# Kernel optimization log

Measured on AMD Instinct MI355X. Metric: run time of the kernel, lower is better.

Reference implementation:

```python
import jax, jax.numpy as jnp
import numpy as np

HEAD_SIZE = 64

def setup_inputs() -> dict:
    key = jax.random.key(0)
    ks = jax.random.split(key, 6)
    B, T, D, H, HS = 4, 2048, 1024, 16, HEAD_SIZE
    s = 1.0 / np.sqrt(D)
    return {
        "x": jax.random.normal(ks[0], (B, T, D), jnp.float32),
        "Wq": jax.random.normal(ks[1], (H, D, HS), jnp.float32) * s,
        "Wk": jax.random.normal(ks[2], (H, D, HS), jnp.float32) * s,
        "Wv": jax.random.normal(ks[3], (H, D, HS), jnp.float32) * s,
        "Wp": jax.random.normal(ks[4], (D, D), jnp.float32) * s,
        "bp": jnp.zeros((D,), jnp.float32),
    }

def reference(x, Wq, Wk, Wv, Wp, bp):
    B, T, D = x.shape
    H, _, HS = Wq.shape
    # per-head projections (bias-free Linears), stacked over heads
    q = jnp.einsum('btd,hde->bhte', x, Wq)
    k = jnp.einsum('btd,hde->bhte', x, Wk)
    v = jnp.einsum('btd,hde->bhte', x, Wv)
    scores = jnp.einsum('bhqe,bhke->bhqk', q, k) / jnp.sqrt(jnp.float32(HS))
    causal = jnp.tril(jnp.ones((T, T), bool))  # mask[:T,:T]
    scores = jnp.where(causal, scores, -jnp.inf)
    w = jax.nn.softmax(scores, axis=-1)  # dropout p=0.0 -> identity
    out = jnp.einsum('bhqk,bhke->bhqe', w, v)
    # concat heads along last dim: [B,T,H*HS] == [B,T,D]
    out = out.transpose(0, 2, 1, 3).reshape(B, T, H * HS)
    return out @ Wp.T + bp  # note: Wp stored as [out,in] like nn.Linear
```

## Files before the change

kernel.cpp:

```cpp
#include <hip/hip_runtime.h>
#include <hip/hip_bf16.h>

typedef unsigned short u16;
typedef unsigned int u32;
typedef __attribute__((ext_vector_type(8))) short short8;
typedef __attribute__((ext_vector_type(4))) float f32x4;

#define B_ 4
#define T_ 2048
#define D_ 1024
#define H_ 16
#define HS_ 64
#define BT (B_*T_)

__device__ __forceinline__ float bf2f(u16 b){ union{u32 u; float f;} v; v.u=((u32)b)<<16; return v.f; }
__device__ __forceinline__ u16 f2bf(float f){
    __hip_bfloat16 h = __float2bfloat16(f);
    union{__hip_bfloat16 h; u16 u;} v; v.h = h; return v.u;
}
__device__ __forceinline__ void split2(float x, u16& h, u16& l){
    u16 hb = f2bf(x);
    float fh = bf2f(hb);
    h = hb; l = f2bf(x - fh);
}
union U4 { u16 s[4]; uint2 v; };
union S8 { u16 s[8]; short8 v; };

#define GLD16(g,l) __builtin_amdgcn_global_load_lds( \
    (__attribute__((address_space(1))) void*)(u16*)(g), \
    (__attribute__((address_space(3))) void*)(l), 16, 0, 0)

__device__ __forceinline__ int swz(int row, int col){
    return row*64 + (((col>>3) ^ (row&7))<<3) + (col&7);
}
#define FCHK(r) (((r)>>1)&3)

#define DPPMV(x, ctrl) __int_as_float(__builtin_amdgcn_update_dpp(0, __float_as_int(x), (ctrl), 0xF, 0xF, true))

__global__ __launch_bounds__(256) void pack_w(const float* __restrict__ Wq,
                                              const float* __restrict__ Wk,
                                              const float* __restrict__ Wv,
                                              u16* __restrict__ Wth,
                                              u16* __restrict__ Wtl)
{
    __shared__ float Tl[64*68];
    const int h = blockIdx.x, dt = blockIdx.y, z = blockIdx.z;
    const float* src = (z==0) ? Wq : ((z==1) ? Wk : Wv);
    const int t = threadIdx.x;
    const int d0 = dt*64;
    #pragma unroll
    for (int i=0;i<4;++i){
        int ci = t + 256*i;
        int dr = ci>>4, ec = ci&15;
        float4 v = *(const float4*)(src + ((size_t)h*D_ + d0+dr)*HS_ + ec*4);
        *(float4*)(Tl + dr*68 + ec*4) = v;
    }
    __syncthreads();
    #pragma unroll
    for (int i=0;i<4;++i){
        int ci = t + 256*i;
        int e = ci>>4, dc = ci&15;
        U4 hh, ll;
        #pragma unroll
        for (int j=0;j<4;++j){
            float f = Tl[(dc*4+j)*68 + e];
            split2(f, hh.s[j], ll.s[j]);
        }
        int n = z*D_ + h*HS_ + e;
        *(uint2*)(Wth + (size_t)n*D_ + d0 + dc*4) = hh.v;
        *(uint2*)(Wtl + (size_t)n*D_ + d0 + dc*4) = ll.v;
    }
}

__global__ __launch_bounds__(256) void gemm_qkv(const float* __restrict__ x,
                                                const u16* __restrict__ Wth,
                                                const u16* __restrict__ Wtl,
                                                float* __restrict__ qo,
                                                u16* __restrict__ kho, u16* __restrict__ klo,
                                                u16* __restrict__ vth, u16* __restrict__ vtl)
{
    __shared__ u16 Ash[128*32], Asl[128*32];
    __shared__ u16 Bsh[128*32], Bsl[128*32];
    const int n0 = blockIdx.x*128, m0 = blockIdx.y*128;
    const int t = threadIdx.x;
    const int w = t>>6, lane = t&63, quad = lane>>4, l16 = lane&15;
    const int wm = (w>>1)*64, wn = (w&1)*64;
    f32x4 acc[4][4];
    #pragma unroll
    for (int i=0;i<4;++i)
        #pragma unroll
        for (int j=0;j<4;++j) acc[i][j] = (f32x4){0.f,0.f,0.f,0.f};
    for (int kt=0; kt<32; ++kt){
        const int k0 = kt*32;
        #pragma unroll
        for (int i=0;i<2;++i){
            int ci = t + 256*i;
            int row = ci>>2, c = ci&3;
            int cs = c ^ FCHK(row);
            GLD16(Wth + (size_t)(n0+row)*D_ + k0 + cs*8, Bsh + ci*8);
            GLD16(Wtl + (size_t)(n0+row)*D_ + k0 + cs*8, Bsl + ci*8);
        }
        #pragma unroll
        for (int i=0;i<4;++i){
            int ci = t + 256*i;
            int row = ci>>3, c4 = ci&7;
            float4 av = *(const float4*)(x + (size_t)(m0+row)*D_ + k0 + c4*4);
            U4 hh, ll;
            split2(av.x, hh.s[0], ll.s[0]); split2(av.y, hh.s[1], ll.s[1]);
            split2(av.z, hh.s[2], ll.s[2]); split2(av.w, hh.s[3], ll.s[3]);
            int off = row*32 + ((((c4>>1) ^ FCHK(row))<<3) | ((c4&1)<<2));
            *(uint2*)(Ash + off) = hh.v;
            *(uint2*)(Asl + off) = ll.v;
        }
        __syncthreads();
        short8 afh[4], afl[4], bfh[4], bfl[4];
        #pragma unroll
        for (int mi=0;mi<4;++mi){
            const int rr = wm+mi*16+l16;
            const int off = rr*32 + ((quad ^ FCHK(rr))<<3);
            afh[mi] = *(const short8*)(Ash + off);
            afl[mi] = *(const short8*)(Asl + off);
        }
        #pragma unroll
        for (int ni=0;ni<4;++ni){
            const int rr = wn+ni*16+l16;
            const int off = rr*32 + ((quad ^ FCHK(rr))<<3);
            bfh[ni] = *(const short8*)(Bsh + off);
            bfl[ni] = *(const short8*)(Bsl + off);
        }
        #pragma unroll
        for (int mi=0;mi<4;++mi)
            #pragma unroll
            for (int ni=0;ni<4;++ni){
                acc[mi][ni] = __builtin_amdgcn_mfma_f32_16x16x32_bf16(afh[mi], bfh[ni], acc[mi][ni], 0,0,0);
                acc[mi][ni] = __builtin_amdgcn_mfma_f32_16x16x32_bf16(afh[mi], bfl[ni], acc[mi][ni], 0,0,0);
                acc[mi][ni] = __builtin_amdgcn_mfma_f32_16x16x32_bf16(afl[mi], bfh[ni], acc[mi][ni], 0,0,0);
            }
        __syncthreads();
    }
    const int z = n0 >> 10;
    if (z == 0){
        #pragma unroll
        for (int ni=0;ni<4;++ni){
            const int nloc = (n0 & 1023) + wn + ni*16 + l16;
            #pragma unroll
            for (int mi=0;mi<4;++mi){
                const int row = m0 + wm + mi*16 + quad*4;
                #pragma unroll
                for (int r=0;r<4;++r)
                    qo[(size_t)(row+r)*D_ + nloc] = acc[mi][ni][r];
            }
        }
    } else if (z == 1){
        #pragma unroll
        for (int ni=0;ni<4;++ni){
            const int nloc = (n0 & 1023) + wn + ni*16 + l16;
            #pragma unroll
            for (int mi=0;mi<4;++mi){
                const int row = m0 + wm + mi*16 + quad*4;
                #pragma unroll
                for (int r=0;r<4;++r){
                    u16 hh, ll; split2(acc[mi][ni][r], hh, ll);
                    kho[(size_t)(row+r)*D_ + nloc] = hh;
                    klo[(size_t)(row+r)*D_ + nloc] = ll;
                }
            }
        }
    } else {
        #pragma unroll
        for (int ni=0;ni<4;++ni){
            const int nloc = (n0 & 1023) + wn + ni*16 + l16;
            const int hloc = nloc>>6, e = nloc&63;
            #pragma unroll
            for (int mi=0;mi<4;++mi){
                const int rowb = m0 + wm + mi*16 + quad*4;
                const int bidx = rowb >> 11, tloc = rowb & 2047;
                U4 hh, ll;
                #pragma unroll
                for (int r=0;r<4;++r) split2(acc[mi][ni][r], hh.s[r], ll.s[r]);
                const size_t adr = ((size_t)((bidx*16 + hloc)*64 + e))*T_ + tloc;
                *(uint2*)(vth + adr) = hh.v;
                *(uint2*)(vtl + adr) = ll.v;
            }
        }
    }
}

__global__ __launch_bounds__(512, 2) void attn(const float* __restrict__ q,
                                            const u16* __restrict__ kh, const u16* __restrict__ kl,
                                            const u16* __restrict__ vth, const u16* __restrict__ vtl,
                                            float* __restrict__ att)
{
    __shared__ u16 Ksh[64*64], Ksl[64*64];
    __shared__ u16 Vsh[64*64], Vsl[64*64];
    __shared__ u16 Pb[8*32*64];
    const int x = blockIdx.y & 7;
    const int bh = (blockIdx.x << 3) | (blockIdx.y >> 3);
    const int b = bh >> 4, h = bh & 15;
    const int t = threadIdx.x;
    const int w = t>>6, lane = t&63, quad = lane>>4, l16 = lane&15;

    u16* Pm = Pb + w*2048;

    const int srow = t>>3, sc = t&7;
    const int slo = swz(srow, sc*8);
    uint4 pkh, pkl, pvh, pvl;
    {
        const size_t gk = ((size_t)(b*T_ + srow))*D_ + h*64 + sc*8;
        pkh = *(const uint4*)(kh + gk);
        pkl = *(const uint4*)(kl + gk);
        const size_t gv = ((size_t)(bh*64 + srow))*T_ + sc*8;
        pvh = *(const uint4*)(vth + gv);
        pvl = *(const uint4*)(vtl + gv);
    }

    #pragma unroll 1
    for (int seg=0; seg<2; ++seg){
        const int qi = seg ? x : (15 - x);
        const int qrow = qi*128 + w*16;

        short8 qh_[2], ql_[2];
        {
            const float* qp = q + ((size_t)(b*T_ + qrow + l16))*D_ + h*64;
            #pragma unroll
            for (int ks=0;ks<2;++ks){
                float4 a0 = *(const float4*)(qp + ks*32 + quad*8);
                float4 a1 = *(const float4*)(qp + ks*32 + quad*8 + 4);
                S8 hh, ll;
                split2(a0.x, hh.s[0], ll.s[0]); split2(a0.y, hh.s[1], ll.s[1]);
                split2(a0.z, hh.s[2], ll.s[2]); split2(a0.w, hh.s[3], ll.s[3]);
                split2(a1.x, hh.s[4], ll.s[4]); split2(a1.y, hh.s[5], ll.s[5]);
                split2(a1.z, hh.s[6], ll.s[6]); split2(a1.w, hh.s[7], ll.s[7]);
                qh_[ks] = hh.v; ql_[ks] = ll.v;
            }
        }
        f32x4 o[4];
        #pragma unroll
        for (int i=0;i<4;++i) o[i] = (f32x4){0.f,0.f,0.f,0.f};
        float m_i[4], l_i[4];
        #pragma unroll
        for (int r=0;r<4;++r){ m_i[r] = -INFINITY; l_i[r] = 0.f; }

        const int kvT = 2*qi + 2;
        for (int kvt=0; kvt<kvT; ++kvt){
            __syncthreads();
            *(uint4*)(Ksh + slo) = pkh;
            *(uint4*)(Ksl + slo) = pkl;
            *(uint4*)(Vsh + slo) = pvh;
            *(uint4*)(Vsl + slo) = pvl;
            const int nk = (kvt+1 < kvT) ? (kvt+1) : ((seg==0) ? 0 : -1);
            if (nk >= 0){
                const size_t gk = ((size_t)(b*T_ + nk*64 + srow))*D_ + h*64 + sc*8;
                pkh = *(const uint4*)(kh + gk);
                pkl = *(const uint4*)(kl + gk);
                const size_t gv = ((size_t)(bh*64 + srow))*T_ + nk*64 + sc*8;
                pvh = *(const uint4*)(vth + gv);
                pvl = *(const uint4*)(vtl + gv);
            }
            __syncthreads();

            float s[4][4];
            __builtin_amdgcn_s_setprio(1);
            #pragma unroll
            for (int ni=0;ni<4;++ni){
                f32x4 sa = (f32x4){0.f,0.f,0.f,0.f};
                const int row = ni*16 + l16;
                #pragma unroll
                for (int ks=0;ks<2;++ks){
                    const int co = swz(row, ks*32 + quad*8);
                    short8 k8h = *(const short8*)(Ksh + co);
                    short8 k8l = *(const short8*)(Ksl + co);
                    sa = __builtin_amdgcn_mfma_f32_16x16x32_bf16(qh_[ks], k8h, sa, 0,0,0);
                    sa = __builtin_amdgcn_mfma_f32_16x16x32_bf16(qh_[ks], k8l, sa, 0,0,0);
                    sa = __builtin_amdgcn_mfma_f32_16x16x32_bf16(ql_[ks], k8h, sa, 0,0,0);
                }
                #pragma unroll
                for (int r=0;r<4;++r) s[ni][r] = sa[r]*0.125f;
            }
            __builtin_amdgcn_s_setprio(0);
            if (kvt*64 + 63 > qrow){
                #pragma unroll
                for (int ni=0;ni<4;++ni){
                    const int colabs = kvt*64 + ni*16 + l16;
                    #pragma unroll
                    for (int r=0;r<4;++r){
                        const int rowabs = qrow + quad*4 + r;
                        if (colabs > rowabs) s[ni][r] = -INFINITY;
                    }
                }
            }
            float alpha[4];
            #pragma unroll
            for (int r=0;r<4;++r){
                float rm = fmaxf(fmaxf(s[0][r],s[1][r]), fmaxf(s[2][r],s[3][r]));
                rm = fmaxf(rm, DPPMV(rm, 0xB1));
                rm = fmaxf(rm, DPPMV(rm, 0x4E));
                rm = fmaxf(rm, DPPMV(rm, 0x124));
                rm = fmaxf(rm, DPPMV(rm, 0x128));
                const float mnew = fmaxf(m_i[r], rm);
                alpha[r] = __expf(m_i[r] - mnew);
                m_i[r] = mnew;
                #pragma unroll
                for (int ni=0;ni<4;++ni) s[ni][r] = __expf(s[ni][r] - mnew);
                float rs = s[0][r]+s[1][r]+s[2][r]+s[3][r];
                rs += DPPMV(rs, 0xB1);
                rs += DPPMV(rs, 0x4E);
                rs += DPPMV(rs, 0x124);
                rs += DPPMV(rs, 0x128);
                l_i[r] = l_i[r]*alpha[r] + rs;
            }
            #pragma unroll
            for (int ni=0;ni<4;++ni)
                #pragma unroll
                for (int r=0;r<4;++r) o[ni][r] *= alpha[r];

            u16 ph[4][4], pl[4][4];
            #pragma unroll
            for (int ni=0;ni<4;++ni)
                #pragma unroll
                for (int r=0;r<4;++r)
                    split2(s[ni][r], ph[ni][r], pl[ni][r]);
            #pragma unroll
            for (int ni=0;ni<4;++ni)
                #pragma unroll
                for (int r=0;r<4;++r){
                    Pm[swz(quad*4+r,      ni*16 + l16)] = ph[ni][r];
                    Pm[swz(16 + quad*4+r, ni*16 + l16)] = pl[ni][r];
                }
            __asm__ volatile("s_waitcnt lgkmcnt(0)" ::: "memory");
            short8 pah[2], pal[2];
            #pragma unroll
            for (int ks=0;ks<2;++ks){
                pah[ks] = *(const short8*)(Pm + swz(l16,      ks*32 + quad*8));
                pal[ks] = *(const short8*)(Pm + swz(16 + l16, ks*32 + quad*8));
            }

            __builtin_amdgcn_s_setprio(1);
            #pragma unroll
            for (int ni=0;ni<4;++ni){
                const int row = ni*16 + l16;
                #pragma unroll
                for (int ks=0;ks<2;++ks){
                    const int co = swz(row, ks*32 + quad*8);
                    short8 v8h = *(const short8*)(Vsh + co);
                    short8 v8l = *(const short8*)(Vsl + co);
                    o[ni] = __builtin_amdgcn_mfma_f32_16x16x32_bf16(pah[ks], v8h, o[ni], 0,0,0);
                    o[ni] = __builtin_amdgcn_mfma_f32_16x16x32_bf16(pah[ks], v8l, o[ni], 0,0,0);
                    o[ni] = __builtin_amdgcn_mfma_f32_16x16x32_bf16(pal[ks], v8h, o[ni], 0,0,0);
                }
            }
            __builtin_amdgcn_s_setprio(0);
        }
        const size_t ob = (size_t)(b*T_ + qrow);
        #pragma unroll
        for (int ni=0;ni<4;++ni){
            const int col = h*64 + ni*16 + l16;
            #pragma unroll
            for (int r=0;r<4;++r)
                att[(ob + quad*4 + r)*D_ + col] = o[ni][r] / l_i[r];
        }
    }
}

__global__ __launch_bounds__(256) void gemm_bt(const float* __restrict__ A,
                                               const float* __restrict__ Bt,
                                               float* __restrict__ C,
                                               const float* __restrict__ bias,
                                               int M, int N, int K)
{
    __shared__ u16 Ash[128*32], Asl[128*32];
    __shared__ u16 Bsh[128*32], Bsl[128*32];
    const int n0 = blockIdx.x*128, m0 = blockIdx.y*128;
    const int t = threadIdx.x;
    const int w = t>>6, lane = t&63, quad = lane>>4, l16 = lane&15;
    const int wm = (w>>1)*64, wn = (w&1)*64;
    f32x4 acc[4][4];
    #pragma unroll
    for (int i=0;i<4;++i)
        #pragma unroll
        for (int j=0;j<4;++j) acc[i][j] = (f32x4){0.f,0.f,0.f,0.f};
    const int kT = K >> 5;
    for (int kt=0; kt<kT; ++kt){
        const int k0 = kt*32;
        #pragma unroll
        for (int i=0;i<4;++i){
            int ci = t + 256*i;
            int row = ci>>3, c4 = ci&7;
            float4 av = *(const float4*)(A  + (size_t)(m0+row)*K + k0 + c4*4);
            float4 bv = *(const float4*)(Bt + (size_t)(n0+row)*K + k0 + c4*4);
            U4 ah, al, bh, bl;
            split2(av.x, ah.s[0], al.s[0]); split2(av.y, ah.s[1], al.s[1]);
            split2(av.z, ah.s[2], al.s[2]); split2(av.w, ah.s[3], al.s[3]);
            split2(bv.x, bh.s[0], bl.s[0]); split2(bv.y, bh.s[1], bl.s[1]);
            split2(bv.z, bh.s[2], bl.s[2]); split2(bv.w, bh.s[3], bl.s[3]);
            int off = row*32 + ((((c4>>1) ^ FCHK(row))<<3) | ((c4&1)<<2));
            *(uint2*)(Ash + off) = ah.v;
            *(uint2*)(Asl + off) = al.v;
            *(uint2*)(Bsh + off) = bh.v;
            *(uint2*)(Bsl + off) = bl.v;
        }
        __syncthreads();
        short8 afh[4], afl[4], bfh[4], bfl[4];
        #pragma unroll
        for (int mi=0;mi<4;++mi){
            const int rr = wm+mi*16+l16;
            const int off = rr*32 + ((quad ^ FCHK(rr))<<3);
            afh[mi] = *(const short8*)(Ash + off);
            afl[mi] = *(const short8*)(Asl + off);
        }
        #pragma unroll
        for (int ni=0;ni<4;++ni){
            const int rr = wn+ni*16+l16;
            const int off = rr*32 + ((quad ^ FCHK(rr))<<3);
            bfh[ni] = *(const short8*)(Bsh + off);
            bfl[ni] = *(const short8*)(Bsl + off);
        }
        #pragma unroll
        for (int mi=0;mi<4;++mi)
            #pragma unroll
            for (int ni=0;ni<4;++ni){
                acc[mi][ni] = __builtin_amdgcn_mfma_f32_16x16x32_bf16(afh[mi], bfh[ni], acc[mi][ni], 0,0,0);
                acc[mi][ni] = __builtin_amdgcn_mfma_f32_16x16x32_bf16(afh[mi], bfl[ni], acc[mi][ni], 0,0,0);
                acc[mi][ni] = __builtin_amdgcn_mfma_f32_16x16x32_bf16(afl[mi], bfh[ni], acc[mi][ni], 0,0,0);
            }
        __syncthreads();
    }
    #pragma unroll
    for (int ni=0;ni<4;++ni){
        const int col = n0 + wn + ni*16 + l16;
        const float bv = bias ? bias[col] : 0.f;
        #pragma unroll
        for (int mi=0;mi<4;++mi){
            const int row = m0 + wm + mi*16 + quad*4;
            #pragma unroll
            for (int r=0;r<4;++r)
                C[(size_t)(row+r)*N + col] = acc[mi][ni][r] + bv;
        }
    }
}

extern "C" void kernel_launch(void* const* d_in, const int* in_sizes, int n_in,
                              void* d_out, int out_size, void* d_ws, size_t ws_size,
                              hipStream_t stream)
{
    const float* x  = (const float*)d_in[0];
    const float* Wq = (const float*)d_in[1];
    const float* Wk = (const float*)d_in[2];
    const float* Wv = (const float*)d_in[3];
    const float* Wp = (const float*)d_in[4];
    const float* bp = (const float*)d_in[5];
    float* out = (float*)d_out;

    float* q   = (float*)d_ws;
    u16*  kh   = (u16*)(q + (size_t)BT*D_);
    u16*  kl   = kh + (size_t)BT*D_;
    u16*  vth  = kl + (size_t)BT*D_;
    u16*  vtl  = vth + (size_t)BT*D_;
    float* att = (float*)(vtl + (size_t)BT*D_);
    u16*  Wth  = (u16*)att;
    u16*  Wtl  = Wth + (size_t)3072*D_;

    pack_w  <<<dim3(16,16,3), 256, 0, stream>>>(Wq, Wk, Wv, Wth, Wtl);
    gemm_qkv<<<dim3(24, BT/128), 256, 0, stream>>>(x, Wth, Wtl, q, kh, kl, vth, vtl);
    attn    <<<dim3(T_/256, B_*H_), 512, 0, stream>>>(q, kh, kl, vth, vtl, att);
    gemm_bt <<<dim3(8, BT/128), 256, 0, stream>>>(att, Wp, out, bp, BT, D_, D_);
}
```

Measured before the change: 493.7 us.

## Pre-split activations and weights into bf16 hi/lo planes for async LDS loads

```diff
diff --git a/kernel.cpp b/kernel.cpp
--- a/kernel.cpp
+++ b/kernel.cpp
@@ -36,6 +36,25 @@
 #define FCHK(r) (((r)>>1)&3)
 
 #define DPPMV(x, ctrl) __int_as_float(__builtin_amdgcn_update_dpp(0, __float_as_int(x), (ctrl), 0xF, 0xF, true))
+
+__global__ __launch_bounds__(256) void split_f32(const float* __restrict__ src,
+                                                 u16* __restrict__ dh, u16* __restrict__ dl,
+                                                 int n8)
+{
+    int i = blockIdx.x*256 + threadIdx.x;
+    const int stride = gridDim.x*256;
+    for (; i < n8; i += stride){
+        float4 a = *(const float4*)(src + (size_t)i*8);
+        float4 b = *(const float4*)(src + (size_t)i*8 + 4);
+        S8 hh, ll;
+        split2(a.x, hh.s[0], ll.s[0]); split2(a.y, hh.s[1], ll.s[1]);
+        split2(a.z, hh.s[2], ll.s[2]); split2(a.w, hh.s[3], ll.s[3]);
+        split2(b.x, hh.s[4], ll.s[4]); split2(b.y, hh.s[5], ll.s[5]);
+        split2(b.z, hh.s[6], ll.s[6]); split2(b.w, hh.s[7], ll.s[7]);
+        *(short8*)(dh + (size_t)i*8) = hh.v;
+        *(short8*)(dl + (size_t)i*8) = ll.v;
+    }
+}
 
 __global__ __launch_bounds__(256) void pack_w(const float* __restrict__ Wq,
                                               const float* __restrict__ Wk,
@@ -72,10 +91,13 @@
     }
 }
 
+template<bool PS>
 __global__ __launch_bounds__(256) void gemm_qkv(const float* __restrict__ x,
+                                                const u16* __restrict__ xh, const u16* __restrict__ xl,
                                                 const u16* __restrict__ Wth,
                                                 const u16* __restrict__ Wtl,
                                                 float* __restrict__ qo,
+                                                u16* __restrict__ qho, u16* __restrict__ qlo,
                                                 u16* __restrict__ kho, u16* __restrict__ klo,
                                                 u16* __restrict__ vth, u16* __restrict__ vtl)
 {
@@ -100,17 +122,28 @@
             GLD16(Wth + (size_t)(n0+row)*D_ + k0 + cs*8, Bsh + ci*8);
             GLD16(Wtl + (size_t)(n0+row)*D_ + k0 + cs*8, Bsl + ci*8);
         }
-        #pragma unroll
-        for (int i=0;i<4;++i){
-            int ci = t + 256*i;
-            int row = ci>>3, c4 = ci&7;
-            float4 av = *(const float4*)(x + (size_t)(m0+row)*D_ + k0 + c4*4);
-            U4 hh, ll;
-            split2(av.x, hh.s[0], ll.s[0]); split2(av.y, hh.s[1], ll.s[1]);
-            split2(av.z, hh.s[2], ll.s[2]); split2(av.w, hh.s[3], ll.s[3]);
-            int off = row*32 + ((((c4>>1) ^ FCHK(row))<<3) | ((c4&1)<<2));
-            *(uint2*)(Ash + off) = hh.v;
-            *(uint2*)(Asl + off) = ll.v;
+        if constexpr(PS){
+            #pragma unroll
+            for (int i=0;i<2;++i){
+                int ci = t + 256*i;
+                int row = ci>>2, c = ci&3;
+                int cs = c ^ FCHK(row);
+                GLD16(xh + (size_t)(m0+row)*D_ + k0 + cs*8, Ash + ci*8);
+                GLD16(xl + (size_t)(m0+row)*D_ + k0 + cs*8, Asl + ci*8);
+            }
+        } else {
+            #pragma unroll
+            for (int i=0;i<4;++i){
+                int ci = t + 256*i;
+                int row = ci>>3, c4 = ci&7;
+                float4 av = *(const float4*)(x + (size_t)(m0+row)*D_ + k0 + c4*4);
+                U4 hh, ll;
+                split2(av.x, hh.s[0], ll.s[0]); split2(av.y, hh.s[1], ll.s[1]);
+                split2(av.z, hh.s[2], ll.s[2]); split2(av.w, hh.s[3], ll.s[3]);
+                int off = row*32 + ((((c4>>1) ^ FCHK(row))<<3) | ((c4&1)<<2));
+                *(uint2*)(Ash + off) = hh.v;
+                *(uint2*)(Asl + off) = ll.v;
+            }
         }
         __syncthreads();
         short8 afh[4], afl[4], bfh[4], bfl[4];
@@ -139,30 +172,51 @@
         __syncthreads();
     }
     const int z = n0 >> 10;
-    if (z == 0){
-        #pragma unroll
-        for (int ni=0;ni<4;++ni){
-            const int nloc = (n0 & 1023) + wn + ni*16 + l16;
-            #pragma unroll
-            for (int mi=0;mi<4;++mi){
-                const int row = m0 + wm + mi*16 + quad*4;
-                #pragma unroll
-                for (int r=0;r<4;++r)
-                    qo[(size_t)(row+r)*D_ + nloc] = acc[mi][ni][r];
-            }
-        }
-    } else if (z == 1){
-        #pragma unroll
-        for (int ni=0;ni<4;++ni){
-            const int nloc = (n0 & 1023) + wn + ni*16 + l16;
-            #pragma unroll
-            for (int mi=0;mi<4;++mi){
-                const int row = m0 + wm + mi*16 + quad*4;
-                #pragma unroll
-                for (int r=0;r<4;++r){
-                    u16 hh, ll; split2(acc[mi][ni][r], hh, ll);
-                    kho[(size_t)(row+r)*D_ + nloc] = hh;
-                    klo[(size_t)(row+r)*D_ + nloc] = ll;
+    if (z <= 1){
+        if constexpr(PS){
+            u16* dh = z ? kho : qho;
+            u16* dl = z ? klo : qlo;
+            #pragma unroll
+            for (int ni=0;ni<4;++ni){
+                const int nloc = (n0 & 1023) + wn + ni*16 + l16;
+                #pragma unroll
+                for (int mi=0;mi<4;++mi){
+                    const int row = m0 + wm + mi*16 + quad*4;
+                    #pragma unroll
+                    for (int r=0;r<4;++r){
+                        u16 hh, ll; split2(acc[mi][ni][r], hh, ll);
+                        dh[(size_t)(row+r)*D_ + nloc] = hh;
+                        dl[(size_t)(row+r)*D_ + nloc] = ll;
+                    }
+                }
+            }
+        } else {
+            if (z == 0){
+                #pragma unroll
+                for (int ni=0;ni<4;++ni){
+                    const int nloc = (n0 & 1023) + wn + ni*16 + l16;
+                    #pragma unroll
+                    for (int mi=0;mi<4;++mi){
+                        const int row = m0 + wm + mi*16 + quad*4;
+                        #pragma unroll
+                        for (int r=0;r<4;++r)
+                            qo[(size_t)(row+r)*D_ + nloc] = acc[mi][ni][r];
+                    }
+                }
+            } else {
+                #pragma unroll
+                for (int ni=0;ni<4;++ni){
+                    const int nloc = (n0 & 1023) + wn + ni*16 + l16;
+                    #pragma unroll
+                    for (int mi=0;mi<4;++mi){
+                        const int row = m0 + wm + mi*16 + quad*4;
+                        #pragma unroll
+                        for (int r=0;r<4;++r){
+                            u16 hh, ll; split2(acc[mi][ni][r], hh, ll);
+                            kho[(size_t)(row+r)*D_ + nloc] = hh;
+                            klo[(size_t)(row+r)*D_ + nloc] = ll;
+                        }
+                    }
                 }
             }
         }
@@ -186,10 +240,13 @@
     }
 }
 
-__global__ __launch_bounds__(512, 2) void attn(const float* __restrict__ q,
+template<bool PS>
+__global__ __launch_bounds__(512, 2) void attn(const float* __restrict__ qf,
+                                            const u16* __restrict__ qh, const u16* __restrict__ ql,
                                             const u16* __restrict__ kh, const u16* __restrict__ kl,
                                             const u16* __restrict__ vth, const u16* __restrict__ vtl,
-                                            float* __restrict__ att)
+                                            float* __restrict__ att,
+                                            u16* __restrict__ atth, u16* __restrict__ attl)
 {
     __shared__ u16 Ksh[64*64], Ksl[64*64];
     __shared__ u16 Vsh[64*64], Vsl[64*64];
@@ -220,8 +277,15 @@
         const int qrow = qi*128 + w*16;
 
         short8 qh_[2], ql_[2];
-        {
-            const float* qp = q + ((size_t)(b*T_ + qrow + l16))*D_ + h*64;
+        if constexpr(PS){
+            const size_t qb = ((size_t)(b*T_ + qrow + l16))*D_ + h*64;
+            #pragma unroll
+            for (int ks=0;ks<2;++ks){
+                qh_[ks] = *(const short8*)(qh + qb + ks*32 + quad*8);
+                ql_[ks] = *(const short8*)(ql + qb + ks*32 + quad*8);
+            }
+        } else {
+            const float* qp = qf + ((size_t)(b*T_ + qrow + l16))*D_ + h*64;
             #pragma unroll
             for (int ks=0;ks<2;++ks){
                 float4 a0 = *(const float4*)(qp + ks*32 + quad*8);
@@ -356,14 +420,25 @@
         for (int ni=0;ni<4;++ni){
             const int col = h*64 + ni*16 + l16;
             #pragma unroll
-            for (int r=0;r<4;++r)
-                att[(ob + quad*4 + r)*D_ + col] = o[ni][r] / l_i[r];
-        }
-    }
-}
-
+            for (int r=0;r<4;++r){
+                const float v = o[ni][r] / l_i[r];
+                const size_t idx = (ob + quad*4 + r)*D_ + col;
+                if constexpr(PS){
+                    u16 hh, ll; split2(v, hh, ll);
+                    atth[idx] = hh; attl[idx] = ll;
+                } else {
+                    att[idx] = v;
+                }
+            }
+        }
+    }
+}
+
+template<bool PS>
 __global__ __launch_bounds__(256) void gemm_bt(const float* __restrict__ A,
+                                               const u16* __restrict__ Ath, const u16* __restrict__ Atl,
                                                const float* __restrict__ Bt,
+                                               const u16* __restrict__ Bth, const u16* __restrict__ Btl,
                                                float* __restrict__ C,
                                                const float* __restrict__ bias,
                                                int M, int N, int K)
@@ -382,22 +457,35 @@
     const int kT = K >> 5;
     for (int kt=0; kt<kT; ++kt){
         const int k0 = kt*32;
-        #pragma unroll
-        for (int i=0;i<4;++i){
-            int ci = t + 256*i;
-            int row = ci>>3, c4 = ci&7;
-            float4 av = *(const float4*)(A  + (size_t)(m0+row)*K + k0 + c4*4);
-            float4 bv = *(const float4*)(Bt + (size_t)(n0+row)*K + k0 + c4*4);
-            U4 ah, al, bh, bl;
-            split2(av.x, ah.s[0], al.s[0]); split2(av.y, ah.s[1], al.s[1]);
-            split2(av.z, ah.s[2], al.s[2]); split2(av.w, ah.s[3], al.s[3]);
-            split2(bv.x, bh.s[0], bl.s[0]); split2(bv.y, bh.s[1], bl.s[1]);
-            split2(bv.z, bh.s[2], bl.s[2]); split2(bv.w, bh.s[3], bl.s[3]);
-            int off = row*32 + ((((c4>>1) ^ FCHK(row))<<3) | ((c4&1)<<2));
-            *(uint2*)(Ash + off) = ah.v;
-            *(uint2*)(Asl + off) = al.v;
-            *(uint2*)(Bsh + off) = bh.v;
-            *(uint2*)(Bsl + off) = bl.v;
+        if constexpr(PS){
+            #pragma unroll
+            for (int i=0;i<2;++i){
+                int ci = t + 256*i;
+                int row = ci>>2, c = ci&3;
+                int cs = c ^ FCHK(row);
+                GLD16(Ath + (size_t)(m0+row)*K + k0 + cs*8, Ash + ci*8);
+                GLD16(Atl + (size_t)(m0+row)*K + k0 + cs*8, Asl + ci*8);
+                GLD16(Bth + (size_t)(n0+row)*K + k0 + cs*8, Bsh + ci*8);
+                GLD16(Btl + (size_t)(n0+row)*K + k0 + cs*8, Bsl + ci*8);
+            }
+        } else {
+            #pragma unroll
+            for (int i=0;i<4;++i){
+                int ci = t + 256*i;
+                int row = ci>>3, c4 = ci&7;
+                float4 av = *(const float4*)(A  + (size_t)(m0+row)*K + k0 + c4*4);
+                float4 bv = *(const float4*)(Bt + (size_t)(n0+row)*K + k0 + c4*4);
+                U4 ah, al, bh, bl;
+                split2(av.x, ah.s[0], al.s[0]); split2(av.y, ah.s[1], al.s[1]);
+                split2(av.z, ah.s[2], al.s[2]); split2(av.w, ah.s[3], al.s[3]);
+                split2(bv.x, bh.s[0], bl.s[0]); split2(bv.y, bh.s[1], bl.s[1]);
+                split2(bv.z, bh.s[2], bl.s[2]); split2(bv.w, bh.s[3], bl.s[3]);
+                int off = row*32 + ((((c4>>1) ^ FCHK(row))<<3) | ((c4&1)<<2));
+                *(uint2*)(Ash + off) = ah.v;
+                *(uint2*)(Asl + off) = al.v;
+                *(uint2*)(Bsh + off) = bh.v;
+                *(uint2*)(Bsl + off) = bl.v;
+            }
         }
         __syncthreads();
         short8 afh[4], afl[4], bfh[4], bfl[4];
@@ -451,17 +539,52 @@
     const float* bp = (const float*)d_in[5];
     float* out = (float*)d_out;
 
-    float* q   = (float*)d_ws;
-    u16*  kh   = (u16*)(q + (size_t)BT*D_);
-    u16*  kl   = kh + (size_t)BT*D_;
-    u16*  vth  = kl + (size_t)BT*D_;
-    u16*  vtl  = vth + (size_t)BT*D_;
-    float* att = (float*)(vtl + (size_t)BT*D_);
-    u16*  Wth  = (u16*)att;
-    u16*  Wtl  = Wth + (size_t)3072*D_;
-
-    pack_w  <<<dim3(16,16,3), 256, 0, stream>>>(Wq, Wk, Wv, Wth, Wtl);
-    gemm_qkv<<<dim3(24, BT/128), 256, 0, stream>>>(x, Wth, Wtl, q, kh, kl, vth, vtl);
-    attn    <<<dim3(T_/256, B_*H_), 512, 0, stream>>>(q, kh, kl, vth, vtl, att);
-    gemm_bt <<<dim3(8, BT/128), 256, 0, stream>>>(att, Wp, out, bp, BT, D_, D_);
-}
+    const size_t NE = (size_t)BT*D_;
+    const size_t NEED = (10*NE + 2*(size_t)D_*D_)*2;
+
+    if (ws_size >= NEED){
+        u16* xh   = (u16*)d_ws;
+        u16* xl   = xh + NE;
+        u16* qh   = xl + NE;
+        u16* ql   = qh + NE;
+        u16* kh   = ql + NE;
+        u16* kl   = kh + NE;
+        u16* vth  = kl + NE;
+        u16* vtl  = vth + NE;
+        u16* atth = vtl + NE;
+        u16* attl = atth + NE;
+        u16* Wph  = attl + NE;
+        u16* Wpl  = Wph + (size_t)D_*D_;
+        u16* Wth  = atth;
+        u16* Wtl  = Wth + (size_t)3072*D_;
+
+        split_f32<<<1024, 256, 0, stream>>>(x,  xh,  xl,  (int)(NE/8));
+        split_f32<<<512,  256, 0, stream>>>(Wp, Wph, Wpl, (int)(((size_t)D_*D_)/8));
+        pack_w   <<<dim3(16,16,3), 256, 0, stream>>>(Wq, Wk, Wv, Wth, Wtl);
+        gemm_qkv<true><<<dim3(24, BT/128), 256, 0, stream>>>(x, xh, xl, Wth, Wtl,
+                                                             nullptr, qh, ql, kh, kl, vth, vtl);
+        attn<true><<<dim3(T_/256, B_*H_), 512, 0, stream>>>(nullptr, qh, ql, kh, kl, vth, vtl,
+                                                            nullptr, atth, attl);
+        gemm_bt<true><<<dim3(8, BT/128), 256, 0, stream>>>(nullptr, atth, attl,
+                                                           nullptr, Wph, Wpl,
+                                                           out, bp, BT, D_, D_);
+    } else {
+        float* q   = (float*)d_ws;
+        u16*  kh   = (u16*)(q + NE);
+        u16*  kl   = kh + NE;
+        u16*  vth  = kl + NE;
+        u16*  vtl  = vth + NE;
+        float* att = (float*)(vtl + NE);
+        u16*  Wth  = (u16*)att;
+        u16*  Wtl  = Wth + (size_t)3072*D_;
+
+        pack_w   <<<dim3(16,16,3), 256, 0, stream>>>(Wq, Wk, Wv, Wth, Wtl);
+        gemm_qkv<false><<<dim3(24, BT/128), 256, 0, stream>>>(x, nullptr, nullptr, Wth, Wtl,
+                                                              q, nullptr, nullptr, kh, kl, vth, vtl);
+        attn<false><<<dim3(T_/256, B_*H_), 512, 0, stream>>>(q, nullptr, nullptr, kh, kl, vth, vtl,
+                                                             att, nullptr, nullptr);
+        gemm_bt<false><<<dim3(8, BT/128), 256, 0, stream>>>(att, nullptr, nullptr,
+                                                            Wp, nullptr, nullptr,
+                                                            out, bp, BT, D_, D_);
+    }
+}
```

Measured after the change: 503.3 us. About the same (+2.0%).

## Halve attention block to 4 waves with 64-row query tiles

Applied to the files above, without the earlier changes.

```diff
diff --git a/kernel.cpp b/kernel.cpp
--- a/kernel.cpp
+++ b/kernel.cpp
@@ -186,42 +186,47 @@
     }
 }
 
-__global__ __launch_bounds__(512, 2) void attn(const float* __restrict__ q,
+__global__ __launch_bounds__(256, 2) void attn(const float* __restrict__ qf,
                                             const u16* __restrict__ kh, const u16* __restrict__ kl,
                                             const u16* __restrict__ vth, const u16* __restrict__ vtl,
                                             float* __restrict__ att)
 {
     __shared__ u16 Ksh[64*64], Ksl[64*64];
     __shared__ u16 Vsh[64*64], Vsl[64*64];
-    __shared__ u16 Pb[8*32*64];
-    const int x = blockIdx.y & 7;
-    const int bh = (blockIdx.x << 3) | (blockIdx.y >> 3);
+    __shared__ u16 Pb[4*16*64];
+    const int bx = blockIdx.x, by = blockIdx.y;
+    const int bh = ((by & 7) << 3) | bx;
+    const int px = by >> 3;
     const int b = bh >> 4, h = bh & 15;
     const int t = threadIdx.x;
     const int w = t>>6, lane = t&63, quad = lane>>4, l16 = lane&15;
 
-    u16* Pm = Pb + w*2048;
-
-    const int srow = t>>3, sc = t&7;
-    const int slo = swz(srow, sc*8);
-    uint4 pkh, pkl, pvh, pvl;
+    u16* Pm = Pb + w*1024;
+
+    const int srow0 = t>>3,        sc0 = t&7;
+    const int srow1 = (t+256)>>3,  sc1 = t&7;
+    const int slo0 = swz(srow0, sc0*8);
+    const int slo1 = swz(srow1, sc1*8);
+    uint4 pkh0, pkh1, pkl0, pkl1, pvh0, pvh1, pvl0, pvl1;
     {
-        const size_t gk = ((size_t)(b*T_ + srow))*D_ + h*64 + sc*8;
-        pkh = *(const uint4*)(kh + gk);
-        pkl = *(const uint4*)(kl + gk);
-        const size_t gv = ((size_t)(bh*64 + srow))*T_ + sc*8;
-        pvh = *(const uint4*)(vth + gv);
-        pvl = *(const uint4*)(vtl + gv);
+        const size_t gk0 = ((size_t)(b*T_ + srow0))*D_ + h*64 + sc0*8;
+        const size_t gk1 = ((size_t)(b*T_ + srow1))*D_ + h*64 + sc1*8;
+        pkh0 = *(const uint4*)(kh + gk0);  pkh1 = *(const uint4*)(kh + gk1);
+        pkl0 = *(const uint4*)(kl + gk0);  pkl1 = *(const uint4*)(kl + gk1);
+        const size_t gv0 = ((size_t)(bh*64 + srow0))*T_ + sc0*8;
+        const size_t gv1 = ((size_t)(bh*64 + srow1))*T_ + sc1*8;
+        pvh0 = *(const uint4*)(vth + gv0); pvh1 = *(const uint4*)(vth + gv1);
+        pvl0 = *(const uint4*)(vtl + gv0); pvl1 = *(const uint4*)(vtl + gv1);
     }
 
     #pragma unroll 1
     for (int seg=0; seg<2; ++seg){
-        const int qi = seg ? x : (15 - x);
-        const int qrow = qi*128 + w*16;
+        const int qi = seg ? px : (31 - px);
+        const int qrow = qi*64 + w*16;
 
         short8 qh_[2], ql_[2];
         {
-            const float* qp = q + ((size_t)(b*T_ + qrow + l16))*D_ + h*64;
+            const float* qp = qf + ((size_t)(b*T_ + qrow + l16))*D_ + h*64;
             #pragma unroll
             for (int ks=0;ks<2;++ks){
                 float4 a0 = *(const float4*)(qp + ks*32 + quad*8);
@@ -241,21 +246,23 @@
         #pragma unroll
         for (int r=0;r<4;++r){ m_i[r] = -INFINITY; l_i[r] = 0.f; }
 
-        const int kvT = 2*qi + 2;
+        const int kvT = qi + 1;
         for (int kvt=0; kvt<kvT; ++kvt){
             __syncthreads();
-            *(uint4*)(Ksh + slo) = pkh;
-            *(uint4*)(Ksl + slo) = pkl;
-            *(uint4*)(Vsh + slo) = pvh;
-            *(uint4*)(Vsl + slo) = pvl;
+            *(uint4*)(Ksh + slo0) = pkh0;  *(uint4*)(Ksh + slo1) = pkh1;
+            *(uint4*)(Ksl + slo0) = pkl0;  *(uint4*)(Ksl + slo1) = pkl1;
+            *(uint4*)(Vsh + slo0) = pvh0;  *(uint4*)(Vsh + slo1) = pvh1;
+            *(uint4*)(Vsl + slo0) = pvl0;  *(uint4*)(Vsl + slo1) = pvl1;
             const int nk = (kvt+1 < kvT) ? (kvt+1) : ((seg==0) ? 0 : -1);
             if (nk >= 0){
-                const size_t gk = ((size_t)(b*T_ + nk*64 + srow))*D_ + h*64 + sc*8;
-                pkh = *(const uint4*)(kh + gk);
-                pkl = *(const uint4*)(kl + gk);
-                const size_t gv = ((size_t)(bh*64 + srow))*T_ + nk*64 + sc*8;
-                pvh = *(const uint4*)(vth + gv);
-                pvl = *(const uint4*)(vtl + gv);
+                const size_t gk0 = ((size_t)(b*T_ + nk*64 + srow0))*D_ + h*64 + sc0*8;
+                const size_t gk1 = ((size_t)(b*T_ + nk*64 + srow1))*D_ + h*64 + sc1*8;
+                pkh0 = *(const uint4*)(kh + gk0);  pkh1 = *(const uint4*)(kh + gk1);
+                pkl0 = *(const uint4*)(kl + gk0);  pkl1 = *(const uint4*)(kl + gk1);
+                const size_t gv0 = ((size_t)(bh*64 + srow0))*T_ + nk*64 + sc0*8;
+                const size_t gv1 = ((size_t)(bh*64 + srow1))*T_ + nk*64 + sc1*8;
+                pvh0 = *(const uint4*)(vth + gv0); pvh1 = *(const uint4*)(vth + gv1);
+                pvl0 = *(const uint4*)(vtl + gv0); pvl1 = *(const uint4*)(vtl + gv1);
             }
             __syncthreads();
 
@@ -323,17 +330,24 @@
             #pragma unroll
             for (int ni=0;ni<4;++ni)
                 #pragma unroll
-                for (int r=0;r<4;++r){
-                    Pm[swz(quad*4+r,      ni*16 + l16)] = ph[ni][r];
-                    Pm[swz(16 + quad*4+r, ni*16 + l16)] = pl[ni][r];
-                }
+                for (int r=0;r<4;++r)
+                    Pm[swz(quad*4+r, ni*16 + l16)] = ph[ni][r];
             __asm__ volatile("s_waitcnt lgkmcnt(0)" ::: "memory");
             short8 pah[2], pal[2];
             #pragma unroll
-            for (int ks=0;ks<2;++ks){
-                pah[ks] = *(const short8*)(Pm + swz(l16,      ks*32 + quad*8));
-                pal[ks] = *(const short8*)(Pm + swz(16 + l16, ks*32 + quad*8));
-            }
+            for (int ks=0;ks<2;++ks)
+                pah[ks] = *(const short8*)(Pm + swz(l16, ks*32 + quad*8));
+            __asm__ volatile("" ::: "memory");
+            #pragma unroll
+            for (int ni=0;ni<4;++ni)
+                #pragma unroll
+                for (int r=0;r<4;++r)
+                    Pm[swz(quad*4+r, ni*16 + l16)] = pl[ni][r];
+            __asm__ volatile("s_waitcnt lgkmcnt(0)" ::: "memory");
+            #pragma unroll
+            for (int ks=0;ks<2;++ks)
+                pal[ks] = *(const short8*)(Pm + swz(l16, ks*32 + quad*8));
+            __asm__ volatile("" ::: "memory");
 
             __builtin_amdgcn_s_setprio(1);
             #pragma unroll
@@ -462,6 +476,6 @@
 
     pack_w  <<<dim3(16,16,3), 256, 0, stream>>>(Wq, Wk, Wv, Wth, Wtl);
     gemm_qkv<<<dim3(24, BT/128), 256, 0, stream>>>(x, Wth, Wtl, q, kh, kl, vth, vtl);
-    attn    <<<dim3(T_/256, B_*H_), 512, 0, stream>>>(q, kh, kl, vth, vtl, att);
+    attn    <<<dim3(8, 128), 256, 0, stream>>>(q, kh, kl, vth, vtl, att);
     gemm_bt <<<dim3(8, BT/128), 256, 0, stream>>>(att, Wp, out, bp, BT, D_, D_);
 }
```

Result: no change. 501.5 us (+1.6%).
